# Kernel tuning notes

Hardware: AMD Instinct MI355X
Metric: run time of the kernel (lower is better)

Reference implementation:

```python
import jax, jax.numpy as jnp
import numpy as np


def _skew(w):
    # w: [B,3] -> [B,3,3] skew-symmetric matrices
    z = jnp.zeros_like(w[:, 0])
    return jnp.stack([
        jnp.stack([z, -w[:, 2], w[:, 1]], axis=-1),
        jnp.stack([w[:, 2], z, -w[:, 0]], axis=-1),
        jnp.stack([-w[:, 1], w[:, 0], z], axis=-1),
    ], axis=-2)


def _twist2mat(w):
    # Rodrigues' formula: exp(skew(w)) for w: [B,3]
    theta = jnp.linalg.norm(w, axis=-1)          # [B]
    safe = jnp.maximum(theta, 1e-12)
    Kx = _skew(w)
    Kx2 = Kx @ Kx
    a = (jnp.sin(theta) / safe)[:, None, None]
    b = ((1.0 - jnp.cos(theta)) / (safe * safe))[:, None, None]
    I = jnp.eye(3, dtype=w.dtype)[None]
    return I + a * Kx + b * Kx2


def setup_inputs():
    key = jax.random.key(0)
    ks = jax.random.split(key, 10)
    B, C, H, W = 64, 8, 120, 160
    N = C * H * W  # 153600
    Jt = 0.01 * jax.random.normal(ks[0], (B, 6, N), dtype=jnp.float32)
    JtJ = jnp.einsum('bin,bjn->bij', Jt, Jt)  # SPD approximated Hessian
    weights = jax.random.uniform(ks[1], (B, C, H, W), dtype=jnp.float32)
    R = 0.1 * jax.random.normal(ks[2], (B, C, H, W), dtype=jnp.float32)
    R0 = _twist2mat(0.2 * jax.random.normal(ks[3], (B, 3), dtype=jnp.float32))
    t0 = jax.random.normal(ks[4], (B, 3, 1), dtype=jnp.float32)
    invD0 = jax.random.uniform(ks[5], (B, 1, H, W), dtype=jnp.float32)
    invD1 = jax.random.uniform(ks[6], (B, 1, H, W), dtype=jnp.float32)
    x0 = jax.random.normal(ks[7], (B, C, H, W), dtype=jnp.float32)
    x1 = jax.random.normal(ks[8], (B, C, H, W), dtype=jnp.float32)
    K = jnp.tile(jnp.array([[120.0, 120.0, 80.0, 60.0]], dtype=jnp.float32), (B, 1))
    return {"JtJ": JtJ, "Jt": Jt, "weights": weights, "R": R, "R0": R0,
            "t0": t0, "invD0": invD0, "invD1": invD1, "x0": x0, "x1": x1, "K": K}


def reference(JtJ, Jt, weights, R, R0, t0, invD0, invD1, x0, x1, K):
    # DirectSolverNet forward, SOLVER_NO_DAMPING branch.
    B = JtJ.shape[0]
    wR = (weights * R).reshape(B, -1, 1)          # [B, N, 1]
    JtR = Jt @ wR                                  # [B, 6, 1]
    eye6 = jnp.eye(6, dtype=JtJ.dtype)[None]       # [1, 6, 6]
    diagJtJ = eye6 * JtJ
    traceJtJ = jnp.sum(diagJtJ, axis=(1, 2))       # [B]
    epsilon = (traceJtJ * 1e-6)[:, None, None] * eye6
    Hessian = JtJ + epsilon
    # inverse_update_pose: invH adds another 1e-6*I regularization
    inv_H = jnp.linalg.inv(Hessian + 1e-6 * eye6)
    xi = inv_H @ JtR                               # [B, 6, 1]
    d_R = _twist2mat(-xi[:, :3, 0])                # [B, 3, 3]
    d_t = -(d_R @ xi[:, 3:])                       # [B, 3, 1]
    # batch_Rt_compose (left multiplication): R_new = R0 @ d_R, t_new = R0 @ d_t + t0
    R_new = R0 @ d_R
    t_new = R0 @ d_t + t0
    return jnp.concatenate([R_new, t_new], axis=2)  # [B, 3, 4] pose
```

## Files before the change

### kernel.cpp

```cpp
#include <hip/hip_runtime.h>


__global__ __launch_bounds__(256) void jtr_kernel(
    const float* __restrict__ Jt,
    const float* __restrict__ w,
    const float* __restrict__ R,
    float* __restrict__ JtR,
    int N) {
  const int b  = blockIdx.y;
  const int n0 = (blockIdx.x * 256 + threadIdx.x) * 4;
  if (n0 >= N) return;

  const float4 wv = *(const float4*)(w + (size_t)b * N + n0);
  const float4 rv = *(const float4*)(R + (size_t)b * N + n0);
  const float4 p  = make_float4(wv.x * rv.x, wv.y * rv.y, wv.z * rv.z, wv.w * rv.w);

  const float* jb = Jt + (size_t)b * 6 * N;
  float acc[6];
#pragma unroll
  for (int i = 0; i < 6; ++i) {
    const float4 jv = *(const float4*)(jb + (size_t)i * N + n0);
    acc[i] = jv.x * p.x + jv.y * p.y + jv.z * p.z + jv.w * p.w;
  }

#pragma unroll
  for (int i = 0; i < 6; ++i) {
    float v = acc[i];
#pragma unroll
    for (int off = 32; off > 0; off >>= 1)
      v += __shfl_down(v, off, 64);
    acc[i] = v;
  }

  __shared__ float part[4][6];
  const int lane = threadIdx.x & 63;
  const int wave = threadIdx.x >> 6;
  if (lane == 0) {
#pragma unroll
    for (int i = 0; i < 6; ++i) part[wave][i] = acc[i];
  }
  __syncthreads();
  if (threadIdx.x < 6) {
    float s = part[0][threadIdx.x] + part[1][threadIdx.x] +
              part[2][threadIdx.x] + part[3][threadIdx.x];
    atomicAdd(&JtR[b * 6 + threadIdx.x], s);
  }
}

__global__ __launch_bounds__(64) void solve_kernel(
    const float* __restrict__ JtJ,
    const float* __restrict__ JtRg,
    const float* __restrict__ R0,
    const float* __restrict__ t0,
    float* __restrict__ out,
    int B) {
  const int b = blockIdx.x * 64 + threadIdx.x;
  if (b >= B) return;

  float H[6][6], rhs[6];
  float tr = 0.0f;
#pragma unroll
  for (int i = 0; i < 6; ++i) {
#pragma unroll
    for (int j = 0; j < 6; ++j) H[i][j] = JtJ[b * 36 + i * 6 + j];
    tr += H[i][i];
  }
  const float eps = tr * 1e-6f + 1e-6f;
#pragma unroll
  for (int i = 0; i < 6; ++i) H[i][i] += eps;
#pragma unroll
  for (int i = 0; i < 6; ++i) rhs[i] = JtRg[b * 6 + i];

#pragma unroll
  for (int k = 0; k < 6; ++k) {
    const float inv = 1.0f / H[k][k];
#pragma unroll
    for (int i = k + 1; i < 6; ++i) {
      const float f = H[i][k] * inv;
#pragma unroll
      for (int j = k + 1; j < 6; ++j) H[i][j] -= f * H[k][j];
      rhs[i] -= f * rhs[k];
    }
  }
  float xi[6];
#pragma unroll
  for (int i = 5; i >= 0; --i) {
    float s = rhs[i];
#pragma unroll
    for (int j = i + 1; j < 6; ++j) s -= H[i][j] * xi[j];
    xi[i] = s / H[i][i];
  }

  const float wx = -xi[0], wy = -xi[1], wz = -xi[2];
  const float th = sqrtf(wx * wx + wy * wy + wz * wz);
  const float safe = fmaxf(th, 1e-12f);
  const float a  = sinf(th) / safe;
  const float bb = (1.0f - cosf(th)) / (safe * safe);

  float K[3][3] = {{0.0f, -wz, wy}, {wz, 0.0f, -wx}, {-wy, wx, 0.0f}};
  float K2[3][3];
#pragma unroll
  for (int r = 0; r < 3; ++r)
#pragma unroll
    for (int c = 0; c < 3; ++c)
      K2[r][c] = K[r][0] * K[0][c] + K[r][1] * K[1][c] + K[r][2] * K[2][c];

  float dR[3][3];
#pragma unroll
  for (int r = 0; r < 3; ++r)
#pragma unroll
    for (int c = 0; c < 3; ++c)
      dR[r][c] = (r == c ? 1.0f : 0.0f) + a * K[r][c] + bb * K2[r][c];

  float dt[3];
#pragma unroll
  for (int r = 0; r < 3; ++r)
    dt[r] = -(dR[r][0] * xi[3] + dR[r][1] * xi[4] + dR[r][2] * xi[5]);

  const float* R0b = R0 + b * 9;
  const float* t0b = t0 + b * 3;
  float* ob = out + b * 12;
#pragma unroll
  for (int r = 0; r < 3; ++r) {
#pragma unroll
    for (int c = 0; c < 3; ++c) {
      ob[r * 4 + c] = R0b[r * 3 + 0] * dR[0][c] +
                      R0b[r * 3 + 1] * dR[1][c] +
                      R0b[r * 3 + 2] * dR[2][c];
    }
    ob[r * 4 + 3] = R0b[r * 3 + 0] * dt[0] +
                    R0b[r * 3 + 1] * dt[1] +
                    R0b[r * 3 + 2] * dt[2] + t0b[r];
  }
}

extern "C" void kernel_launch(void* const* d_in, const int* in_sizes, int n_in,
                              void* d_out, int out_size, void* d_ws, size_t ws_size,
                              hipStream_t stream) {
  const float* JtJ = (const float*)d_in[0];
  const float* Jt  = (const float*)d_in[1];
  const float* w   = (const float*)d_in[2];
  const float* R   = (const float*)d_in[3];
  const float* R0  = (const float*)d_in[4];
  const float* t0  = (const float*)d_in[5];
  float* out = (float*)d_out;

  const int B = in_sizes[0] / 36;
  const int N = in_sizes[1] / (6 * B);

  float* JtR = (float*)d_ws;
  hipMemsetAsync(JtR, 0, (size_t)B * 6 * sizeof(float), stream);

  const int elemsPerBlock = 256 * 4;
  dim3 grid((N + elemsPerBlock - 1) / elemsPerBlock, B);
  jtr_kernel<<<grid, 256, 0, stream>>>(Jt, w, R, JtR, N);

  solve_kernel<<<(B + 63) / 64, 64, 0, stream>>>(JtJ, JtR, R0, t0, out, B);
}
```

Measured before the change: 413.7 us.

## Replace atomic JtR reduction with per-block partials and nontemporal 2x-wide loads

Each thread now handles two float4 chunks and reads them with nontemporal loads. The block count halves to N/2048 per batch. Instead of atomically adding into a memset workspace, each block writes its partial sums to a per-block slot. The solve kernel then runs one block per batch item and reduces those partials in shared memory before a single thread solves. This removes the memset launch and the atomic contention, at the cost of assuming N is divisible by 2048 and serialising the solve per block.

```diff
diff --git a/kernel.cpp b/kernel.cpp
--- a/kernel.cpp
+++ b/kernel.cpp
@@ -1,26 +1,36 @@
 #include <hip/hip_runtime.h>
 
+
+typedef float vfloat4 __attribute__((ext_vector_type(4)));
 
 __global__ __launch_bounds__(256) void jtr_kernel(
     const float* __restrict__ Jt,
     const float* __restrict__ w,
     const float* __restrict__ R,
-    float* __restrict__ JtR,
-    int N) {
-  const int b  = blockIdx.y;
-  const int n0 = (blockIdx.x * 256 + threadIdx.x) * 4;
-  if (n0 >= N) return;
+    float* __restrict__ part,
+    int N, int gx) {
+  const int b    = blockIdx.y;
+  const int base = blockIdx.x * 2048;
+  const int t4   = threadIdx.x * 4;
+  const size_t bN = (size_t)b * N;
+  const int n0 = base + t4;
+  const int n1 = base + 1024 + t4;
 
-  const float4 wv = *(const float4*)(w + (size_t)b * N + n0);
-  const float4 rv = *(const float4*)(R + (size_t)b * N + n0);
-  const float4 p  = make_float4(wv.x * rv.x, wv.y * rv.y, wv.z * rv.z, wv.w * rv.w);
+  const vfloat4 w0 = __builtin_nontemporal_load((const vfloat4*)(w + bN + n0));
+  const vfloat4 w1 = __builtin_nontemporal_load((const vfloat4*)(w + bN + n1));
+  const vfloat4 r0 = __builtin_nontemporal_load((const vfloat4*)(R + bN + n0));
+  const vfloat4 r1 = __builtin_nontemporal_load((const vfloat4*)(R + bN + n1));
+  const vfloat4 p0 = w0 * r0;
+  const vfloat4 p1 = w1 * r1;
 
-  const float* jb = Jt + (size_t)b * 6 * N;
+  const float* jb = Jt + bN * 6;
   float acc[6];
 #pragma unroll
   for (int i = 0; i < 6; ++i) {
-    const float4 jv = *(const float4*)(jb + (size_t)i * N + n0);
-    acc[i] = jv.x * p.x + jv.y * p.y + jv.z * p.z + jv.w * p.w;
+    const vfloat4 j0 = __builtin_nontemporal_load((const vfloat4*)(jb + (size_t)i * N + n0));
+    const vfloat4 j1 = __builtin_nontemporal_load((const vfloat4*)(jb + (size_t)i * N + n1));
+    const vfloat4 s = j0 * p0 + j1 * p1;
+    acc[i] = s.x + s.y + s.z + s.w;
   }
 
 #pragma unroll
@@ -32,44 +42,63 @@
     acc[i] = v;
   }
 
-  __shared__ float part[4][6];
+  __shared__ float ws[4][6];
   const int lane = threadIdx.x & 63;
   const int wave = threadIdx.x >> 6;
   if (lane == 0) {
 #pragma unroll
-    for (int i = 0; i < 6; ++i) part[wave][i] = acc[i];
+    for (int i = 0; i < 6; ++i) ws[wave][i] = acc[i];
   }
   __syncthreads();
   if (threadIdx.x < 6) {
-    float s = part[0][threadIdx.x] + part[1][threadIdx.x] +
-              part[2][threadIdx.x] + part[3][threadIdx.x];
-    atomicAdd(&JtR[b * 6 + threadIdx.x], s);
+    part[((size_t)b * gx + blockIdx.x) * 6 + threadIdx.x] =
+        ws[0][threadIdx.x] + ws[1][threadIdx.x] +
+        ws[2][threadIdx.x] + ws[3][threadIdx.x];
   }
 }
 
 __global__ __launch_bounds__(64) void solve_kernel(
     const float* __restrict__ JtJ,
-    const float* __restrict__ JtRg,
+    const float* __restrict__ part,
     const float* __restrict__ R0,
     const float* __restrict__ t0,
     float* __restrict__ out,
-    int B) {
-  const int b = blockIdx.x * 64 + threadIdx.x;
-  if (b >= B) return;
+    int gx) {
+  const int b = blockIdx.x;
+  const int t = threadIdx.x;
+  __shared__ float lds[10][6];
+  __shared__ float jtr[6];
+
+  if (t < 60) {
+    const int r = t % 6, k = t / 6;
+    float s = 0.0f;
+    for (int j = k; j < gx; j += 10)
+      s += part[((size_t)b * gx + j) * 6 + r];
+    lds[k][r] = s;
+  }
+  __syncthreads();
+  if (t < 6) {
+    float s = 0.0f;
+#pragma unroll
+    for (int k = 0; k < 10; ++k) s += lds[k][t];
+    jtr[t] = s;
+  }
+  __syncthreads();
+  if (t != 0) return;
 
   float H[6][6], rhs[6];
-  float tr = 0.0f;
+  float trace = 0.0f;
 #pragma unroll
   for (int i = 0; i < 6; ++i) {
 #pragma unroll
     for (int j = 0; j < 6; ++j) H[i][j] = JtJ[b * 36 + i * 6 + j];
-    tr += H[i][i];
+    trace += H[i][i];
   }
-  const float eps = tr * 1e-6f + 1e-6f;
+  const float eps = trace * 1e-6f + 1e-6f;
 #pragma unroll
   for (int i = 0; i < 6; ++i) H[i][i] += eps;
 #pragma unroll
-  for (int i = 0; i < 6; ++i) rhs[i] = JtRg[b * 6 + i];
+  for (int i = 0; i < 6; ++i) rhs[i] = jtr[i];
 
 #pragma unroll
   for (int k = 0; k < 6; ++k) {
@@ -97,7 +126,7 @@
   const float a  = sinf(th) / safe;
   const float bb = (1.0f - cosf(th)) / (safe * safe);
 
-  float K[3][3] = {{0.0f, -wz, wy}, {wz, 0.0f, -wx}, {-wy, wx, 0.0f}};
+  const float K[3][3] = {{0.0f, -wz, wy}, {wz, 0.0f, -wx}, {-wy, wx, 0.0f}};
   float K2[3][3];
 #pragma unroll
   for (int r = 0; r < 3; ++r)
@@ -147,13 +176,11 @@
 
   const int B = in_sizes[0] / 36;
   const int N = in_sizes[1] / (6 * B);
+  const int gx = N / 2048;
 
-  float* JtR = (float*)d_ws;
-  hipMemsetAsync(JtR, 0, (size_t)B * 6 * sizeof(float), stream);
+  float* part = (float*)d_ws;
 
-  const int elemsPerBlock = 256 * 4;
-  dim3 grid((N + elemsPerBlock - 1) / elemsPerBlock, B);
-  jtr_kernel<<<grid, 256, 0, stream>>>(Jt, w, R, JtR, N);
-
-  solve_kernel<<<(B + 63) / 64, 64, 0, stream>>>(JtJ, JtR, R0, t0, out, B);
+  dim3 grid(gx, B);
+  jtr_kernel<<<grid, 256, 0, stream>>>(Jt, w, R, part, N, gx);
+  solve_kernel<<<B, 64, 0, stream>>>(JtJ, part, R0, t0, out, gx);
 }
```

Result: faster. 392.5 us (-5.1%).
